# Performance work log

Measured on AMD Instinct MI355X. Metric: run time of the kernel, lower is better.

The kernel has to match this reference:

```python
import jax, jax.numpy as jnp
import numpy as np
from jax import lax

B, S, D, H, L = 2, 2048, 512, 512, 2
M, NC, K, NH, WIN = 64, 16, 4, 8, 256
MAX_LR = 0.1


def setup_inputs() -> dict:
    key = jax.random.key(0)
    keys = iter(jax.random.split(key, 40))
    def nrm(shape, scale=0.02):
        return jax.random.normal(next(keys), shape, dtype=jnp.float32) * scale
    p = {}
    p['x'] = jax.random.normal(next(keys), (B, S, D), dtype=jnp.float32)
    p['meta_memory'] = nrm((M, D), 0.05)
    p['mem_w_in'] = nrm((D, H)); p['mem_b_in'] = jnp.zeros((H,))
    p['mem_w_h'] = nrm((L, H, H)); p['mem_b_h'] = jnp.zeros((L, H))
    p['mem_w_out'] = nrm((H, D)); p['mem_b_out'] = jnp.zeros((D,))
    for n in ('w_in', 'b_in', 'w_h', 'b_h', 'w_out', 'b_out'):
        p['mom_' + n] = jnp.zeros_like(p['mem_' + n])
    for pre in ('q', 'k', 'v'):
        p[pre + '_w'] = nrm((D, D)); p[pre + '_b'] = jnp.zeros((D,))
        p[pre + '_conv'] = nrm((D, 1, K), 0.1)
    for pre in ('lr', 'fg', 'mo'):
        p[pre + '_w'] = nrm((D, 1)); p[pre + '_b'] = jnp.zeros((1,))
    for n in ('swa_wq', 'swa_wk', 'swa_wv', 'swa_wo'):
        p[n] = nrm((D, D))
    for n in ('swa_bq', 'swa_bk', 'swa_bv', 'swa_bo'):
        p[n] = jnp.zeros((D,))
    return p


def l2n(x):
    # F.normalize(x, dim=-1): x / max(||x||_2, 1e-12)
    return x / jnp.maximum(jnp.linalg.norm(x, axis=-1, keepdims=True), 1e-12)


def causal_dwconv(x, kernel):
    # x [B,S,D], kernel [D,1,K] depthwise causal conv along S
    xc = jnp.transpose(x, (0, 2, 1))  # [B,D,S]
    y = lax.conv_general_dilated(xc, kernel, window_strides=(1,), padding=[(K - 1, 0)],
                                 feature_group_count=D, dimension_numbers=('NCH', 'OIH', 'NCH'))
    return jnp.transpose(y, (0, 2, 1))


def lin_proj(x, W, b, conv, n_chunks):
    # Linear -> causal depthwise conv -> SiLU -> chunk: [B, n_chunks, S/n_chunks, D]
    y = jax.nn.silu(causal_dwconv(x @ W + b, conv))
    Bx, Sx, Dx = y.shape
    return y.reshape(Bx, n_chunks, Sx // n_chunks, Dx)


def adaptive(x, W, b, max_w):
    # data-dependent scalar gate in (0, max_w], chunked: [B, NC, chunk_len, 1]
    y = jax.nn.sigmoid(x @ W + b) * max_w
    Bx, Sx, _ = y.shape
    return y.reshape(Bx, NC, Sx // NC, 1)


def mlp(params, x):
    # ResLinear: in-proj + SiLU, residual SiLU hidden layers, out-proj
    h = jax.nn.silu(x @ params['w_in'] + params['b_in'])
    def body(h, wb):
        w, b = wb
        return h + jax.nn.silu(h @ w + b), None
    h, _ = lax.scan(body, h, (params['w_h'], params['b_h']))
    return h @ params['w_out'] + params['b_out']


def swa_attn(x, wq, bq, wk, bk, wv, bv, wo, bo):
    Bx, Sx, Dx = x.shape
    hd = Dx // NH
    def split(y):
        return jnp.transpose(y.reshape(Bx, Sx, NH, hd), (0, 2, 1, 3))
    q, k, v = split(x @ wq + bq), split(x @ wk + bk), split(x @ wv + bv)
    scores = jnp.einsum('bhqd,bhkd->bhqk', q, k) / np.sqrt(hd).astype(np.float32)
    i = jnp.arange(Sx)[:, None]
    j = jnp.arange(Sx)[None, :]
    mask = (j <= i) & (i - j < WIN)  # causal sliding window
    attn = jax.nn.softmax(jnp.where(mask, scores, jnp.float32(-1e9)), axis=-1)
    out = jnp.einsum('bhqk,bhkd->bhqd', attn, v)
    out = jnp.transpose(out, (0, 2, 1, 3)).reshape(Bx, Sx, Dx)
    return out @ wo + bo


def reference(x, meta_memory, mem_w_in, mem_b_in, mem_w_h, mem_b_h, mem_w_out, mem_b_out,
              mom_w_in, mom_b_in, mom_w_h, mom_b_h, mom_w_out, mom_b_out,
              q_w, q_b, q_conv, k_w, k_b, k_conv, v_w, v_b, v_conv,
              lr_w, lr_b, fg_w, fg_b, mo_w, mo_b,
              swa_wq, swa_bq, swa_wk, swa_bk, swa_wv, swa_bv, swa_wo, swa_bo):
    Bx = x.shape[0]
    # inject meta memory; (M+S) chosen divisible by NC so no padding branch
    xm = jnp.concatenate([jnp.broadcast_to(meta_memory, (Bx, M, D)), x], axis=1)
    q = l2n(lin_proj(xm, q_w, q_b, q_conv, 1))      # [B,1,M+S,D]
    k = l2n(lin_proj(xm, k_w, k_b, k_conv, NC))     # [B,NC,C,D]
    v = lin_proj(xm, v_w, v_b, v_conv, NC)
    lr = adaptive(xm, lr_w, lr_b, MAX_LR)           # [B,NC,C,1]
    fg = adaptive(xm, fg_w, fg_b, 1.0)
    mo = adaptive(xm, mo_w, mo_b, 1.0)
    params = {'w_in': mem_w_in, 'b_in': mem_b_in, 'w_h': mem_w_h, 'b_h': mem_b_h,
              'w_out': mem_w_out, 'b_out': mem_b_out}
    moms = {'w_in': mom_w_in, 'b_in': mom_b_in, 'w_h': mom_w_h, 'b_h': mom_b_h,
            'w_out': mom_w_out, 'b_out': mom_b_out}

    def loss_fn(p, kc, vc, lrc):
        preds = mlp(p, kc)                           # [B,C,D]
        loss = jnp.mean((preds - vc) ** 2, axis=-1)  # [B,C]
        return jnp.sum(loss * lrc[..., 0]), loss

    grads, _ = jax.vmap(jax.grad(loss_fn, has_aux=True), in_axes=(None, 1, 1, 1))(params, k, v, lr)
    alpha = fg.mean(axis=(1, 2, 3))  # [B]
    theta = lr.mean(axis=(1, 2, 3))
    eta = mo.mean(axis=(1, 2, 3))
    new_params = {}
    for name, p_ in params.items():
        g = grads[name].mean(axis=0)                # mean over chunks
        sh = (-1,) + (1,) * g.ndim                  # flatten_and_expand
        mom_b = eta.reshape(sh) * moms[name] - theta.reshape(sh) * g   # [B,*shape]
        # torch updates param.data under no_grad -> stop_gradient for faithfulness
        new_params[name] = lax.stop_gradient((p_ * (1.0 - alpha.reshape(sh)) + mom_b).mean(axis=0))
    retrieved = jax.nn.silu(mlp(new_params, q[:, 0]))
    out = swa_attn(retrieved, swa_wq, swa_bq, swa_wk, swa_bk, swa_wv, swa_bv, swa_wo, swa_bo)
    return out[:, M:, :]
```

## Files before the change

### kernel.cpp

```cpp
#include <hip/hip_runtime.h>
#include <cmath>


namespace {

constexpr int Bb   = 2;
constexpr int Ss   = 2048;
constexpr int Dd   = 512;
constexpr int Mm   = 64;
constexpr int NCc  = 16;
constexpr int NHh  = 8;
constexpr int HD   = 64;
constexpr int WINw = 256;
constexpr int Nn   = Mm + Ss;
constexpr int Rr   = Bb * Nn;
constexpr int NBD  = Rr * Dd;
constexpr float MAXLR = 0.1f;
constexpr float GS   = 256.0f;

typedef __attribute__((ext_vector_type(8))) short short8;
typedef __attribute__((ext_vector_type(8))) _Float16 half8;
typedef __attribute__((ext_vector_type(4))) float f32x4;

__device__ __forceinline__ float sigf(float x)  { return 1.0f / (1.0f + __expf(-x)); }
__device__ __forceinline__ float siluf(float x) { return x * sigf(x); }
__device__ __forceinline__ float dsiluf(float x){ float s = sigf(x); return s * (1.0f + x * (1.0f - s)); }
__device__ __forceinline__ unsigned short f2h(float f) {
    _Float16 h = (_Float16)f;
    return *(unsigned short*)&h;
}
__device__ __forceinline__ float h2f(unsigned short u) {
    return (float)(*(_Float16*)&u);
}
// ... 73 lines not shown
        unsigned short nh16[16];
        #pragma unroll
        for (int e = 0; e < 16; ++e) nh16[e] = f2h(vals[e]);
        unsigned short* np = wc.nh[seg] + (size_t)(r0 + tr) * 512 + c0 + tc;
        *(short8*)np = *(short8*)nh16; *(short8*)(np + 8) = *(short8*)(nh16 + 8);
    }
    __syncthreads();
    int c = threadIdx.x >> 2, rb = (threadIdx.x & 3) * 16;
    unsigned short o16[16];
    #pragma unroll
    for (int e = 0; e < 16; ++e) o16[e] = f2h(T[rb + e][c]);
    unsigned short* tp = wc.th[seg] + (size_t)(c0 + c) * 512 + r0 + rb;
    *(short8*)tp = *(short8*)o16; *(short8*)(tp + 8) = *(short8*)(o16 + 8);
}

struct TriW { const unsigned short* bh; const float* bias; float* c; };
struct TriSet { TriW t[3]; };

template<int TA, int TB, bool SPLITK, int EPI, bool MULTI, bool AF32>
__global__ __launch_bounds__(256) void k_mm(
        const void* Ap, const unsigned short* Bh_,
        float* C, const float* bias, const float* __restrict__ exf,
        const unsigned short* __restrict__ exh,
        const float* __restrict__ lrp,
        unsigned short* oh, TriSet ts,
        int Md, int Nd, int Kd, int accum) {
    __shared__ char smem[16384];
    unsigned short* AH = (unsigned short*)smem;
    unsigned short* BH = AH + 4096;
    const int tid = threadIdx.x;
    const int m0 = blockIdx.x * 64, n0 = blockIdx.y * 64;
    if constexpr (MULTI) {
        const TriW& tw = ts.t[blockIdx.z];
        Bh_ = tw.bh; bias = tw.bias; C = tw.c;
    }
    int kbg = 0, ke = Kd;
    if constexpr (SPLITK) {
        int kc = Kd / gridDim.z;
        kbg = blockIdx.z * kc; ke = kbg + kc;
        C += (size_t)blockIdx.z * Md * Nd;
    }
    const int astr = (TA == 0) ? Kd : Md;

    f32x4 acc[2][2];
    #pragma unroll
    for (int i = 0; i < 2; ++i)
        #pragma unroll
        for (int j = 0; j < 2; ++j)
            #pragma unroll
            for (int v = 0; v < 4; ++v) acc[i][j][v] = 0.f;

    short8 pA0, pA1, pB0, pB1;
    float4 pAf[4];

    auto gload = [&](int k0) {
        if constexpr (TA == 0) {
            int r = tid >> 2, ks2 = (tid & 3) * 16;
            if constexpr (AF32) {
                const float* ap = (const float*)Ap + (size_t)(m0 + r) * astr + k0 + ks2;
                pAf[0] = *(const float4*)ap;       pAf[1] = *(const float4*)(ap + 4);
                pAf[2] = *(const float4*)(ap + 8); pAf[3] = *(const float4*)(ap + 12);
            } else {
                const unsigned short* ah = (const unsigned short*)Ap + (size_t)(m0 + r) * astr + k0 + ks2;
                pA0 = *(const short8*)ah; pA1 = *(const short8*)(ah + 8);
            }
        } else {
            int kr = tid >> 2, ms = (tid & 3) * 16;
            const unsigned short* ah = (const unsigned short*)Ap + (size_t)(k0 + kr) * astr + m0 + ms;
            pA0 = *(const short8*)ah; pA1 = *(const short8*)(ah + 8);
        }
        if constexpr (TB == 0) {
            int nr = tid >> 2, ks2 = (tid & 3) * 16;
            const unsigned short* bh = Bh_ + (size_t)(n0 + nr) * Kd + k0 + ks2;
            pB0 = *(const short8*)bh; pB1 = *(const short8*)(bh + 8);
        } else {
            int kr = tid >> 2, nseg = (tid & 3) * 16;
            const unsigned short* bh = Bh_ + (size_t)(k0 + kr) * Nd + n0 + nseg;
            pB0 = *(const short8*)bh; pB1 = *(const short8*)(bh + 8);
        }
    };
    auto lstore = [&]() {
        if constexpr (TA == 0) {
            int r = tid >> 2, ks2 = (tid & 3) * 16;
            int f = r >> 4, rr = r & 15, kf = ks2 >> 5, q = (ks2 >> 3) & 3;
            int F = (f * 2 + kf) * 4 + q;
            int u0 = swz(F * 16 + rr) * 8, u1 = swz((F + 1) * 16 + rr) * 8;
            if constexpr (AF32) {
                unsigned short hh[16];
                const float* pf = (const float*)pAf;
                #pragma unroll
                for (int e = 0; e < 16; ++e) hh[e] = f2h(pf[e]);
                *(short8*)(AH + u0) = *(short8*)hh;  *(short8*)(AH + u1) = *(short8*)(hh + 8);
            } else {
                *(short8*)(AH + u0) = pA0; *(short8*)(AH + u1) = pA1;
            }
        } else {
            int kr = tid >> 2, ms = (tid & 3) * 16;
            int f = ms >> 4, kf = kr >> 5, q = (kr >> 3) & 3, kk = kr & 7;
            int F = (f * 2 + kf) * 4 + q;
            unsigned short tmp[16];
            *(short8*)tmp = pA0; *(short8*)(tmp + 8) = pA1;
            #pragma unroll
            for (int e = 0; e < 16; ++e) AH[swz((F << 4) | e) * 8 + kk] = tmp[e];
        }
        if constexpr (TB == 0) {
            int nr = tid >> 2, ks2 = (tid & 3) * 16;
            int f = nr >> 4, rr = nr & 15, kf = ks2 >> 5, q = (ks2 >> 3) & 3;
            int F = (f * 2 + kf) * 4 + q;
            int u0 = swz(F * 16 + rr) * 8, u1 = swz((F + 1) * 16 + rr) * 8;
            *(short8*)(BH + u0) = pB0; *(short8*)(BH + u1) = pB1;
        } else {
            int kr = tid >> 2, nseg = (tid & 3) * 16;
            int f = nseg >> 4, kf = kr >> 5, q = (kr >> 3) & 3, kk = kr & 7;
            int F = (f * 2 + kf) * 4 + q;
            unsigned short tmp[16];
            *(short8*)tmp = pB0; *(short8*)(tmp + 8) = pB1;
            #pragma unroll
            for (int e = 0; e < 16; ++e) BH[swz((F << 4) | e) * 8 + kk] = tmp[e];
        }
    };

    const int wv = tid >> 6, lr16 = tid & 15, lq = (tid >> 4) & 3;
    const int wm = wv & 1, wn = wv >> 1;

    gload(kbg); lstore();
    __syncthreads();
    for (int k0 = kbg; k0 < ke; k0 += 64) {
        bool more = (k0 + 64) < ke;
        if (more) gload(k0 + 64);
        #pragma unroll
        for (int kf = 0; kf < 2; ++kf) {
            half8 fa[2], fb[2];
            #pragma unroll
            for (int i = 0; i < 2; ++i) {
                int u = swz((((wm * 2 + i) * 2 + kf) * 4 + lq) * 16 + lr16);
                fa[i] = *(const half8*)(AH + u * 8);
            }
            #pragma unroll
            for (int j = 0; j < 2; ++j) {
                int u = swz((((wn * 2 + j) * 2 + kf) * 4 + lq) * 16 + lr16);
                fb[j] = *(const half8*)(BH + u * 8);
            }
            #pragma unroll
            for (int i = 0; i < 2; ++i)
                #pragma unroll
                for (int j = 0; j < 2; ++j)
                    acc[i][j] = __builtin_amdgcn_mfma_f32_16x16x32_f16(fa[i], fb[j], acc[i][j], 0, 0, 0);
        }
        if (more) { __syncthreads(); lstore(); __syncthreads(); }
    }
    __syncthreads();

    float* EP = (float*)smem;
    #pragma unroll
    for (int i = 0; i < 2; ++i)
        #pragma unroll
// ... 4 lines not shown
                int col = wn * 32 + j * 16 + lr16;
                int u = col >> 2, up = u ^ (row & 15);
                EP[row * 64 + up * 4 + (col & 3)] = acc[i][j][v];
            }
    __syncthreads();
    int r = tid >> 2, cg = tid & 3;
    float vv[16];
    #pragma unroll
    for (int uu = 0; uu < 4; ++uu) {
        int u = cg * 4 + uu;
        *(float4*)&vv[uu * 4] = *(const float4*)&EP[r * 64 + ((u ^ (r & 15)) * 4)];
    }
    int m = m0 + r, nb = n0 + cg * 16;
    size_t idx = (size_t)m * Nd + nb;

    if constexpr (SPLITK) {
        #pragma unroll
        for (int uu = 0; uu < 4; ++uu) *(float4*)(C + idx + uu * 4) = *(float4*)&vv[uu * 4];
        return;
    }
    if (bias) {
        #pragma unroll
        for (int uu = 0; uu < 4; ++uu) {
            float4 b4 = *(const float4*)(bias + nb + uu * 4);
            vv[uu * 4 + 0] += b4.x; vv[uu * 4 + 1] += b4.y;
            vv[uu * 4 + 2] += b4.z; vv[uu * 4 + 3] += b4.w;
        }
    }
    unsigned short eh8[16];
    if constexpr (EPI == 2 || EPI == 3 || EPI == 6) {
        #pragma unroll
        for (int k4 = 0; k4 < 2; ++k4)
            *(short8*)&eh8[k4 * 8] = *(const short8*)(exh + idx + k4 * 8);
    }
    auto store_h = [&](const float* s) {
        unsigned short hb[16];
        #pragma unroll
        for (int e = 0; e < 16; ++e) hb[e] = f2h(s[e]);
        *(short8*)(oh + idx) = *(short8*)hb;
        *(short8*)(oh + idx + 8) = *(short8*)(hb + 8);
    };
    auto accum_add = [&]() {
        #pragma unroll
        for (int uu = 0; uu < 4; ++uu) {
            float4 o4 = *(const float4*)(C + idx + uu * 4);
            vv[uu * 4 + 0] += o4.x; vv[uu * 4 + 1] += o4.y;
            vv[uu * 4 + 2] += o4.z; vv[uu * 4 + 3] += o4.w;
        }
    };
    auto store_f = [&]() {
        #pragma unroll
        for (int uu = 0; uu < 4; ++uu) *(float4*)(C + idx + uu * 4) = *(float4*)&vv[uu * 4];
    };
    if constexpr (EPI == 0) {
        if (accum) accum_add();
        store_f();
    } else if constexpr (EPI == 1) {
        float s[16];
        #pragma unroll
        for (int e = 0; e < 16; ++e) s[e] = siluf(vv[e]);
        store_h(s);
    } else if constexpr (EPI == 2) {
        float s[16];
        #pragma unroll
        for (int e = 0; e < 16; ++e) s[e] = h2f(eh8[e]) + siluf(vv[e]);
        store_h(s);
    } else if constexpr (EPI == 3) {
        float sc = GS * (2.0f / 512.0f) * lrp[m];
        float s[16];
        #pragma unroll
        for (int e = 0; e < 16; ++e) s[e] = sc * (vv[e] - h2f(eh8[e]));
        store_h(s);
    } else if constexpr (EPI == 4) {
        if (accum) accum_add();
        store_f();
        float s[16];
        #pragma unroll
        for (int e = 0; e < 16; ++e) s[e] = vv[e] * dsiluf(exf[idx + e]);
        store_h(s);
    } else if constexpr (EPI == 5) {
        store_f();
        float s[16];
        #pragma unroll
        for (int e = 0; e < 16; ++e) s[e] = siluf(vv[e]);
        store_h(s);
    } else if constexpr (EPI == 6) {
        store_f();
        float s[16];
        #pragma unroll
        for (int e = 0; e < 16; ++e) s[e] = h2f(eh8[e]) + siluf(vv[e]);
        store_h(s);
    } else if constexpr (EPI == 7) {
        int b2 = m / Nn, t2 = m - b2 * Nn;
        if (t2 >= Mm) {
            float* dst = C + (size_t)(b2 * Ss + (t2 - Mm)) * Nd + nb;
            #pragma unroll
            for (int uu = 0; uu < 4; ++uu) *(float4*)(dst + uu * 4) = *(float4*)&vv[uu * 4];
        }
    }
}

__global__ void k_reduce_splitk(const float* __restrict__ part, float* __restrict__ out,
                                int n, int z, float alpha) {
    int i = blockIdx.x * 256 + threadIdx.x;
    if (i >= n) return;
    float s = 0.f;
    for (int zz = 0; zz < z; ++zz) s += part[(size_t)zz * n + i];
    out[i] = alpha * s;
}

__global__ __launch_bounds__(256) void k_conv3(
        const float* __restrict__ yq, const float* __restrict__ yk, const float* __restrict__ yv,
        const float* __restrict__ cq, const float* __restrict__ ck, const float* __restrict__ cv,
        unsigned short* oq, unsigned short* ok, unsigned short* ov) {
    int which = blockIdx.y;
    const float* y  = which == 0 ? yq : which == 1 ? yk : yv;
    const float* cw = which == 0 ? cq : which == 1 ? ck : cv;
    unsigned short* oh = which == 0 ? oq : which == 1 ? ok : ov;
    bool norm = which < 2;
    int r = blockIdx.x;
    int b = r / Nn, t = r - b * Nn;
    const size_t rowbase = (size_t)r * Dd;
    float s[2];
    #pragma unroll
    for (int u = 0; u < 2; ++u) {
        int d = threadIdx.x + u * 256;
        float acc = 0.f;
        #pragma unroll
        for (int k = 0; k < 4; ++k) {
            int tt = t - 3 + k;
            if (tt >= 0) acc += y[(size_t)(b * Nn + tt) * Dd + d] * cw[d * 4 + k];
        }
        s[u] = siluf(acc);
    }
    float denom = 1.0f;
    if (norm) {
        __shared__ float wr[4];
        float v2 = s[0] * s[0] + s[1] * s[1];
        #pragma unroll
        for (int off = 32; off; off >>= 1) v2 += __shfl_xor(v2, off, 64);
        if ((threadIdx.x & 63) == 0) wr[threadIdx.x >> 6] = v2;
        __syncthreads();
        denom = fmaxf(sqrtf(wr[0] + wr[1] + wr[2] + wr[3]), 1e-12f);
    }
    oh[rowbase + threadIdx.x]       = f2h(s[0] / denom);
    oh[rowbase + threadIdx.x + 256] = f2h(s[1] / denom);
}

__global__ void k_colsum(const unsigned short* __restrict__ gh, float* __restrict__ part) {
    int col = blockIdx.x * 256 + threadIdx.x;
    int chunk = blockIdx.y;
    int r0 = chunk * (Rr / 64);
    float s = 0.f;
    for (int r = r0; r < r0 + Rr / 64; ++r) s += h2f(gh[(size_t)r * Dd + col]);
    part[chunk * Dd + col] = s;
}
__global__ void k_colsum_reduce(const float* __restrict__ part, float* __restrict__ out, float alpha) {
    int col = blockIdx.x * 256 + threadIdx.x;
    if (col >= Dd) return;
    float s = 0.f;
    for (int c = 0; c < 64; ++c) s += part[c * Dd + col];
    out[col] = alpha * s;
}

struct UpdW4 { const float* p[4]; const float* mo[4]; const float* g[4]; unsigned short* th[4]; };
__global__ __launch_bounds__(256) void k_updW(UpdW4 u, const float* __restrict__ scal) {
    __shared__ float T[64][65];
    int seg = blockIdx.z;
    int r0 = blockIdx.y * 64, c0 = blockIdx.x * 64;
    float a = 1.0f - scal[0], et = scal[2], th = scal[1];
    int tr = threadIdx.x >> 2, tc = (threadIdx.x & 3) * 16;
    size_t base = (size_t)(r0 + tr) * 512 + c0 + tc;
    #pragma unroll
    for (int q = 0; q < 4; ++q) {
        float4 p4 = *(const float4*)(u.p[seg] + base + q * 4);
        float4 m4 = *(const float4*)(u.mo[seg] + base + q * 4);
        float4 g4 = *(const float4*)(u.g[seg] + base + q * 4);
// ... 5 lines not shown
    __syncthreads();
    int c = threadIdx.x >> 2, rb = (threadIdx.x & 3) * 16;
    unsigned short o16[16];
    #pragma unroll
    for (int e = 0; e < 16; ++e) o16[e] = f2h(T[rb + e][c]);
    unsigned short* tp = u.th[seg] + (size_t)(c0 + c) * 512 + r0 + rb;
    *(short8*)tp = *(short8*)o16; *(short8*)(tp + 8) = *(short8*)(o16 + 8);
}
struct UpdB4 { const float* p[4]; const float* mo[4]; const float* g[4]; float* o[4]; };
__global__ void k_updB(UpdB4 u, const float* __restrict__ scal) {
    int seg = blockIdx.x >> 1;
    int i = (blockIdx.x & 1) * 256 + threadIdx.x;
    u.o[seg][i] = u.p[seg][i] * (1.0f - scal[0]) + scal[2] * u.mo[seg][i] - scal[1] * u.g[seg][i];
}

__global__ __launch_bounds__(256) void k_swa(const float* __restrict__ qs,
                                             const float* __restrict__ ks,
                                             const float* __restrict__ vs,
                                             float* __restrict__ out) {
    __shared__ unsigned short KH[2048], VH[2048];
    __shared__ unsigned short PH[4][512];
    const int tid = threadIdx.x;
    const int w = tid >> 6, lane = tid & 63;
    const int lq = lane >> 4, l16 = lane & 15;
    const int q0 = blockIdx.x * 64;
    const int bh = blockIdx.y;
    const int h = bh & 7, b = bh >> 3;
    const size_t srow = (size_t)(b * Nn) * Dd + h * HD;
    const int iq = q0 + w * 16 + l16;

    half8 qh[2];
    {
        const float* qr = qs + srow + (size_t)iq * Dd;
        #pragma unroll
        for (int kf = 0; kf < 2; ++kf) {
            float t8[8];
            *(float4*)&t8[0] = *(const float4*)(qr + kf * 32 + lq * 8);
            *(float4*)&t8[4] = *(const float4*)(qr + kf * 32 + lq * 8 + 4);
            unsigned short hh[8];
            #pragma unroll
            for (int e = 0; e < 8; ++e) hh[e] = f2h(t8[e]);
            qh[kf] = *(half8*)hh;
        }
    }

    f32x4 o[4];
    #pragma unroll
    for (int nf = 0; nf < 4; ++nf)
        #pragma unroll
        for (int v = 0; v < 4; ++v) o[nf][v] = 0.f;
    float mrun[4] = { -1e30f, -1e30f, -1e30f, -1e30f };
    float lrun[4] = { 0.f, 0.f, 0.f, 0.f };
    const int iw = q0 + w * 16 + lq * 4;

    int jlo = q0 - (WINw - 1); if (jlo < 0) jlo = 0;
    jlo &= ~31;
    for (int jt = jlo; jt < q0 + 64; jt += 32) {
        __syncthreads();
        {
            int nr = tid >> 3, ds8 = (tid & 7) * 8;
            const float* kr = ks + srow + (size_t)(jt + nr) * Dd + ds8;
            float t8[8];
            *(float4*)&t8[0] = *(const float4*)kr;
            *(float4*)&t8[4] = *(const float4*)(kr + 4);
            unsigned short hh[8];
            #pragma unroll
            for (int e = 0; e < 8; ++e) hh[e] = f2h(t8[e]);
            int f = nr >> 4, rr = nr & 15, kf = ds8 >> 5, q = (ds8 >> 3) & 3;
            int u = swz(((f * 2 + kf) * 4 + q) * 16 + rr);
            *(short8*)(KH + u * 8) = *(short8*)hh;
        }
        {
            int d = tid & 63, kg = tid >> 6;
            unsigned short hh[8];
            #pragma unroll
            for (int e = 0; e < 8; ++e)
                hh[e] = f2h(vs[srow + (size_t)(jt + kg * 8 + e) * Dd + d]);
            int f = d >> 4, rr = d & 15;
            int u = swz((f * 4 + kg) * 16 + rr);
            *(short8*)(VH + u * 8) = *(short8*)hh;
        }
        __syncthreads();

        f32x4 s[2];
        #pragma unroll
        for (int nf = 0; nf < 2; ++nf) {
            #pragma unroll
            for (int v = 0; v < 4; ++v) s[nf][v] = 0.f;
            #pragma unroll
            for (int kf = 0; kf < 2; ++kf) {
                int u = swz(((nf * 2 + kf) * 4 + lq) * 16 + l16);
                half8 kb = *(const half8*)(KH + u * 8);
// ... 47 lines not shown
        half8 pah = *(const half8*)(&PH[w][pa]);
        #pragma unroll
        for (int nf = 0; nf < 4; ++nf) {
            int u = swz((nf * 4 + lq) * 16 + l16);
            half8 vth = *(const half8*)(VH + u * 8);
            o[nf] = __builtin_amdgcn_mfma_f32_16x16x32_f16(pah, vth, o[nf], 0, 0, 0);
        }
    }
    float invl[4];
    #pragma unroll
    for (int v = 0; v < 4; ++v) invl[v] = 1.0f / lrun[v];
    #pragma unroll
    for (int nf = 0; nf < 4; ++nf)
        #pragma unroll
        for (int v = 0; v < 4; ++v)
            out[srow + (size_t)(iw + v) * Dd + nf * 16 + l16] = o[nf][v] * invl[v];
}

}

extern "C" void kernel_launch(void* const* d_in, const int* in_sizes, int n_in,
                              void* d_out, int out_size, void* d_ws, size_t ws_size,
                              hipStream_t stream) {
    const float* x       = (const float*)d_in[0];
    const float* meta    = (const float*)d_in[1];
    const float* mWin    = (const float*)d_in[2];
    const float* mbin    = (const float*)d_in[3];
    const float* mWh     = (const float*)d_in[4];
    const float* mbh     = (const float*)d_in[5];
    const float* mWout   = (const float*)d_in[6];
    const float* mbout   = (const float*)d_in[7];
// ... 17 lines not shown

    char* wsb = (char*)d_ws;
    size_t off = 0;
    auto allocB = [&](size_t bytes) { void* p = wsb + off; off = (off + bytes + 255) & ~(size_t)255; return p; };
    auto allocU = [&](size_t elems) { return (unsigned short*)allocB(elems * 2); };
    auto allocF = [&](size_t elems) { return (float*)allocB(elems * 4); };

    unsigned short *xm_h = allocU(NBD);
    unsigned short *qb_h = allocU(NBD);
    unsigned short *kb_h = allocU(NBD);
    unsigned short *vb_h = allocU(NBD);
    unsigned short *h0_h = allocU(NBD);
    unsigned short *h1_h = allocU(NBD);
    unsigned short *h2_h = allocU(NBD);
    unsigned short *g1_h = allocU(NBD);
    float *f0 = allocF(NBD), *f1 = allocF(NBD), *f2 = allocF(NBD), *f3 = allocF(NBD);
    float *parts = allocF((size_t)12 * 262144);
    const int WEL = 262144;
    unsigned short *wt_h[11], *wn_h[11];
    for (int i = 0; i < 11; ++i) { wt_h[i] = allocU(WEL); wn_h[i] = nullptr; }
    for (int i = 8; i < 11; ++i) wn_h[i] = allocU(WEL);
    unsigned short *nWinT_h = allocU(WEL);
    unsigned short *nWh0T_h = allocU(WEL);
    unsigned short *nWh1T_h = allocU(WEL);
    unsigned short *nWoutT_h = allocU(WEL);
    float *gWin = allocF(WEL), *gWh0 = allocF(WEL), *gWh1 = allocF(WEL), *gWout = allocF(WEL);
    float *gbin = allocF(512), *gbh0 = allocF(512), *gbh1 = allocF(512), *gbout = allocF(512);
    float *nbin = allocF(512), *nbh0 = allocF(512), *nbh1 = allocF(512), *nbout = allocF(512);
    float *lr_t = allocF(Rr), *fg_t = allocF(Rr), *mo_t = allocF(Rr);
    float *scal = allocF(8);
    float *cpart = allocF(64 * 512);
    unsigned short *gA_h = vb_h;
    unsigned short *gB_h = xm_h;

    TriSet none{};
    const dim3 GG(66, 8);
    const float GALPHA = 1.0f / (NCc * GS);

    WC wc{};
    const float* wlist[11] = { q_w, k_w, v_w, swa_wq, swa_wk, swa_wv, swa_wo,
                               mWin, mWh, mWh + WEL, mWout };
    for (int i = 0; i < 11; ++i) { wc.w[i] = wlist[i]; wc.th[i] = wt_h[i]; wc.nh[i] = wn_h[i]; }
    k_wconv<<<dim3(8, 8, 11), 256, 0, stream>>>(wc);

    k_build_xm<<<(Rr * 128 + 255) / 256, 256, 0, stream>>>(x, meta, xm_h);
    k_gates<<<Rr / 4, 256, 0, stream>>>(xm_h, lr_w, lr_b, fg_w, fg_b, mo_w, mo_b, lr_t, fg_t, mo_t);
    k_gate_means<<<1, 256, 0, stream>>>(lr_t, fg_t, mo_t, scal);

    TriSet qkvA{{ { wt_h[0], q_b, f0 }, { wt_h[1], k_b, f1 }, { wt_h[2], v_b, f2 } }};
    k_mm<0, 0, false, 0, true, false><<<dim3(66, 8, 3), 256, 0, stream>>>(
        xm_h, nullptr, nullptr, nullptr, nullptr, nullptr, nullptr, nullptr, qkvA, Rr, Dd, Dd, 0);
    k_conv3<<<dim3(Rr, 3), 256, 0, stream>>>(f0, f1, f2, q_c, k_c, v_c, qb_h, kb_h, vb_h);

    k_mm<0, 0, false, 5, false, false><<<GG, 256, 0, stream>>>(
        kb_h, wt_h[7], f0, mbin, nullptr, nullptr, nullptr, h0_h, none, Rr, Dd, Dd, 0);
    k_mm<0, 0, false, 6, false, false><<<GG, 256, 0, stream>>>(
        h0_h, wt_h[8], f1, mbh, nullptr, h0_h, nullptr, h1_h, none, Rr, Dd, Dd, 0);
    k_mm<0, 0, false, 6, false, false><<<GG, 256, 0, stream>>>(
        h1_h, wt_h[9], f2, mbh + 512, nullptr, h1_h, nullptr, h2_h, none, Rr, Dd, Dd, 0);
    k_mm<0, 0, false, 3, false, false><<<GG, 256, 0, stream>>>(
        h2_h, wt_h[10], nullptr, mbout, nullptr, vb_h, lr_t, g1_h, none, Rr, Dd, Dd, 0);

    auto GRADW = [&](const unsigned short* ah, const unsigned short* bh, float* gout) {
        k_mm<1, 1, true, 0, false, false><<<dim3(8, 8, 11), 256, 0, stream>>>(
            ah, bh, parts, nullptr, nullptr, nullptr, nullptr, nullptr, none, Dd, Dd, Rr, 0);
        k_reduce_splitk<<<1024, 256, 0, stream>>>(parts, gout, WEL, 11, GALPHA);
    };
    auto COLSUM = [&](const unsigned short* gh, float* bo) {
        k_colsum<<<dim3(2, 64), 256, 0, stream>>>(gh, cpart);
        k_colsum_reduce<<<2, 256, 0, stream>>>(cpart, bo, GALPHA);
    };
    GRADW(h2_h, g1_h, gWout);  COLSUM(g1_h, gbout);
    k_mm<0, 0, false, 4, false, false><<<GG, 256, 0, stream>>>(
        g1_h, wn_h[10], f3, nullptr, f2, nullptr, nullptr, gA_h, none, Rr, Dd, Dd, 0);
    GRADW(h1_h, gA_h, gWh1);   COLSUM(gA_h, gbh1);
    k_mm<0, 0, false, 4, false, false><<<GG, 256, 0, stream>>>(
        gA_h, wn_h[9], f3, nullptr, f1, nullptr, nullptr, gB_h, none, Rr, Dd, Dd, 1);
    GRADW(h0_h, gB_h, gWh0);   COLSUM(gB_h, gbh0);
    k_mm<0, 0, false, 4, false, false><<<GG, 256, 0, stream>>>(
        gB_h, wn_h[8], f3, nullptr, f0, nullptr, nullptr, gA_h, none, Rr, Dd, Dd, 1);
    GRADW(kb_h, gA_h, gWin);   COLSUM(gA_h, gbin);

    UpdW4 uw{ { mWin, mWh, mWh + WEL, mWout },
              { momWin, momWh, momWh + WEL, momWout },
              { gWin, gWh0, gWh1, gWout },
              { nWinT_h, nWh0T_h, nWh1T_h, nWoutT_h } };
    k_updW<<<dim3(8, 8, 4), 256, 0, stream>>>(uw, scal);
    UpdB4 ub{ { mbin, mbh, mbh + 512, mbout },
              { mombin, mombh, mombh + 512, mombout },
              { gbin, gbh0, gbh1, gbout },
              { nbin, nbh0, nbh1, nbout } };
    k_updB<<<8, 256, 0, stream>>>(ub, scal);

    k_mm<0, 0, false, 1, false, false><<<GG, 256, 0, stream>>>(
        qb_h, nWinT_h, nullptr, nbin, nullptr, nullptr, nullptr, g1_h, none, Rr, Dd, Dd, 0);
    k_mm<0, 0, false, 2, false, false><<<GG, 256, 0, stream>>>(
        g1_h, nWh0T_h, nullptr, nbh0, nullptr, g1_h, nullptr, h0_h, none, Rr, Dd, Dd, 0);
    k_mm<0, 0, false, 2, false, false><<<GG, 256, 0, stream>>>(
        h0_h, nWh1T_h, nullptr, nbh1, nullptr, h0_h, nullptr, h1_h, none, Rr, Dd, Dd, 0);
    k_mm<0, 0, false, 1, false, false><<<GG, 256, 0, stream>>>(
        h1_h, nWoutT_h, nullptr, nbout, nullptr, nullptr, nullptr, h2_h, none, Rr, Dd, Dd, 0);

    TriSet qkvF{{ { wt_h[3], swa_bq, f0 }, { wt_h[4], swa_bk, f1 }, { wt_h[5], swa_bv, f2 } }};
    k_mm<0, 0, false, 0, true, false><<<dim3(66, 8, 3), 256, 0, stream>>>(
        h2_h, nullptr, nullptr, nullptr, nullptr, nullptr, nullptr, nullptr, qkvF, Rr, Dd, Dd, 0);
    k_swa<<<dim3(Nn / 64, Bb * NHh), 256, 0, stream>>>(f0, f1, f2, f3);
    k_mm<0, 0, false, 7, false, true><<<GG, 256, 0, stream>>>(
        f3, wt_h[6], (float*)d_out, swa_bo, nullptr, nullptr, nullptr, nullptr, none, Rr, Dd, Dd, 0);
}
```

Measured before the change: 512.5 us.

## Store intermediates in fp16, batch weight-gradient GEMMs, load B fragments directly

```diff
diff --git a/kernel.cpp b/kernel.cpp
--- a/kernel.cpp
+++ b/kernel.cpp
@@ -17,6 +17,7 @@
 constexpr int NBD  = Rr * Dd;
 constexpr float MAXLR = 0.1f;
 constexpr float GS   = 256.0f;
+constexpr int WEL  = 262144;
 
 typedef __attribute__((ext_vector_type(8))) short short8;
 typedef __attribute__((ext_vector_type(8))) _Float16 half8;
@@ -120,16 +121,18 @@
     *(short8*)tp = *(short8*)o16; *(short8*)(tp + 8) = *(short8*)(o16 + 8);
 }
 
-struct TriW { const unsigned short* bh; const float* bias; float* c; };
+struct TriW { const unsigned short* bh; const float* bias; unsigned short* ch; };
 struct TriSet { TriW t[3]; };
-
-template<int TA, int TB, bool SPLITK, int EPI, bool MULTI, bool AF32>
+struct Grad4 { const unsigned short* a[4]; const unsigned short* b[4]; };
+
+template<int TA, int TB, bool SPLITK, int EPI, bool MULTI, bool GRAD4>
 __global__ __launch_bounds__(256) void k_mm(
-        const void* Ap, const unsigned short* Bh_,
-        float* C, const float* bias, const float* __restrict__ exf,
-        const unsigned short* __restrict__ exh,
+        const unsigned short* Ap, const unsigned short* Bh_,
+        float* C, const float* bias,
+        const unsigned short* __restrict__ exA,
+        const unsigned short* __restrict__ exD,
         const float* __restrict__ lrp,
-        unsigned short* oh, TriSet ts,
+        unsigned short* oh, unsigned short* oh2, TriSet ts, Grad4 g4,
         int Md, int Nd, int Kd, int accum) {
     __shared__ char smem[16384];
     unsigned short* AH = (unsigned short*)smem;
@@ -138,10 +141,15 @@
     const int m0 = blockIdx.x * 64, n0 = blockIdx.y * 64;
     if constexpr (MULTI) {
         const TriW& tw = ts.t[blockIdx.z];
-        Bh_ = tw.bh; bias = tw.bias; C = tw.c;
+        Bh_ = tw.bh; bias = tw.bias; oh = tw.ch;
     }
     int kbg = 0, ke = Kd;
-    if constexpr (SPLITK) {
+    if constexpr (GRAD4) {
+        int seg = blockIdx.z / 11, kz = blockIdx.z - seg * 11;
+        kbg = kz * 384; ke = kbg + 384;
+        C += (size_t)blockIdx.z * Md * Nd;
+        Ap = g4.a[seg]; Bh_ = g4.b[seg];
+    } else if constexpr (SPLITK) {
         int kc = Kd / gridDim.z;
         kbg = blockIdx.z * kc; ke = kbg + kc;
         C += (size_t)blockIdx.z * Md * Nd;
@@ -157,29 +165,24 @@
             for (int v = 0; v < 4; ++v) acc[i][j][v] = 0.f;
 
     short8 pA0, pA1, pB0, pB1;
-    float4 pAf[4];
+
+    const int wv = tid >> 6, lr16 = tid & 15, lq = (tid >> 4) & 3;
+    const int wm = wv & 1, wn = wv >> 1;
+    const unsigned short* bdir = nullptr;
+    if constexpr (TB == 0)
+        bdir = Bh_ + (size_t)(n0 + wn * 32 + lr16) * Kd + lq * 8;
 
     auto gload = [&](int k0) {
         if constexpr (TA == 0) {
             int r = tid >> 2, ks2 = (tid & 3) * 16;
-            if constexpr (AF32) {
-                const float* ap = (const float*)Ap + (size_t)(m0 + r) * astr + k0 + ks2;
-                pAf[0] = *(const float4*)ap;       pAf[1] = *(const float4*)(ap + 4);
-                pAf[2] = *(const float4*)(ap + 8); pAf[3] = *(const float4*)(ap + 12);
-            } else {
-                const unsigned short* ah = (const unsigned short*)Ap + (size_t)(m0 + r) * astr + k0 + ks2;
-                pA0 = *(const short8*)ah; pA1 = *(const short8*)(ah + 8);
-            }
+            const unsigned short* ah = Ap + (size_t)(m0 + r) * astr + k0 + ks2;
+            pA0 = *(const short8*)ah; pA1 = *(const short8*)(ah + 8);
         } else {
             int kr = tid >> 2, ms = (tid & 3) * 16;
-            const unsigned short* ah = (const unsigned short*)Ap + (size_t)(k0 + kr) * astr + m0 + ms;
+            const unsigned short* ah = Ap + (size_t)(k0 + kr) * astr + m0 + ms;
             pA0 = *(const short8*)ah; pA1 = *(const short8*)(ah + 8);
         }
-        if constexpr (TB == 0) {
-            int nr = tid >> 2, ks2 = (tid & 3) * 16;
-            const unsigned short* bh = Bh_ + (size_t)(n0 + nr) * Kd + k0 + ks2;
-            pB0 = *(const short8*)bh; pB1 = *(const short8*)(bh + 8);
-        } else {
+        if constexpr (TB == 1) {
             int kr = tid >> 2, nseg = (tid & 3) * 16;
             const unsigned short* bh = Bh_ + (size_t)(k0 + kr) * Nd + n0 + nseg;
             pB0 = *(const short8*)bh; pB1 = *(const short8*)(bh + 8);
@@ -191,15 +194,7 @@
             int f = r >> 4, rr = r & 15, kf = ks2 >> 5, q = (ks2 >> 3) & 3;
             int F = (f * 2 + kf) * 4 + q;
             int u0 = swz(F * 16 + rr) * 8, u1 = swz((F + 1) * 16 + rr) * 8;
-            if constexpr (AF32) {
-                unsigned short hh[16];
-                const float* pf = (const float*)pAf;
-                #pragma unroll
-                for (int e = 0; e < 16; ++e) hh[e] = f2h(pf[e]);
-                *(short8*)(AH + u0) = *(short8*)hh;  *(short8*)(AH + u1) = *(short8*)(hh + 8);
-            } else {
-                *(short8*)(AH + u0) = pA0; *(short8*)(AH + u1) = pA1;
-            }
+            *(short8*)(AH + u0) = pA0; *(short8*)(AH + u1) = pA1;
         } else {
             int kr = tid >> 2, ms = (tid & 3) * 16;
             int f = ms >> 4, kf = kr >> 5, q = (kr >> 3) & 3, kk = kr & 7;
@@ -209,13 +204,7 @@
             #pragma unroll
             for (int e = 0; e < 16; ++e) AH[swz((F << 4) | e) * 8 + kk] = tmp[e];
         }
-        if constexpr (TB == 0) {
-            int nr = tid >> 2, ks2 = (tid & 3) * 16;
-            int f = nr >> 4, rr = nr & 15, kf = ks2 >> 5, q = (ks2 >> 3) & 3;
-            int F = (f * 2 + kf) * 4 + q;
-            int u0 = swz(F * 16 + rr) * 8, u1 = swz((F + 1) * 16 + rr) * 8;
-            *(short8*)(BH + u0) = pB0; *(short8*)(BH + u1) = pB1;
-        } else {
+        if constexpr (TB == 1) {
             int kr = tid >> 2, nseg = (tid & 3) * 16;
             int f = nseg >> 4, kf = kr >> 5, q = (kr >> 3) & 3, kk = kr & 7;
             int F = (f * 2 + kf) * 4 + q;
@@ -226,14 +215,19 @@
         }
     };
 
-    const int wv = tid >> 6, lr16 = tid & 15, lq = (tid >> 4) & 3;
-    const int wm = wv & 1, wn = wv >> 1;
-
     gload(kbg); lstore();
     __syncthreads();
     for (int k0 = kbg; k0 < ke; k0 += 64) {
         bool more = (k0 + 64) < ke;
         if (more) gload(k0 + 64);
+        half8 gb[2][2];
+        if constexpr (TB == 0) {
+            #pragma unroll
+            for (int kf = 0; kf < 2; ++kf)
+                #pragma unroll
+                for (int j = 0; j < 2; ++j)
+                    gb[kf][j] = *(const half8*)(bdir + (size_t)j * 16 * Kd + k0 + kf * 32);
+        }
         #pragma unroll
         for (int kf = 0; kf < 2; ++kf) {
             half8 fa[2], fb[2];
@@ -244,8 +238,11 @@
             }
             #pragma unroll
             for (int j = 0; j < 2; ++j) {
-                int u = swz((((wn * 2 + j) * 2 + kf) * 4 + lq) * 16 + lr16);
-                fb[j] = *(const half8*)(BH + u * 8);
+                if constexpr (TB == 0) fb[j] = gb[kf][j];
+                else {
+                    int u = swz((((wn * 2 + j) * 2 + kf) * 4 + lq) * 16 + lr16);
+                    fb[j] = *(const half8*)(BH + u * 8);
+                }
             }
             #pragma unroll
             for (int i = 0; i < 2; ++i)
@@ -280,7 +277,7 @@
     int m = m0 + r, nb = n0 + cg * 16;
     size_t idx = (size_t)m * Nd + nb;
 
-    if constexpr (SPLITK) {
+    if constexpr (SPLITK || GRAD4) {
         #pragma unroll
         for (int uu = 0; uu < 4; ++uu) *(float4*)(C + idx + uu * 4) = *(float4*)&vv[uu * 4];
         return;
@@ -293,11 +290,10 @@
             vv[uu * 4 + 2] += b4.z; vv[uu * 4 + 3] += b4.w;
         }
     }
-    unsigned short eh8[16];
+    unsigned short ea[16];
     if constexpr (EPI == 2 || EPI == 3 || EPI == 6) {
-        #pragma unroll
-        for (int k4 = 0; k4 < 2; ++k4)
-            *(short8*)&eh8[k4 * 8] = *(const short8*)(exh + idx + k4 * 8);
+        *(short8*)&ea[0] = *(const short8*)(exA + idx);
+        *(short8*)&ea[8] = *(const short8*)(exA + idx + 8);
     }
     auto store_h = [&](const float* s) {
         unsigned short hb[16];
@@ -306,21 +302,24 @@
         *(short8*)(oh + idx) = *(short8*)hb;
         *(short8*)(oh + idx + 8) = *(short8*)(hb + 8);
     };
-    auto accum_add = [&]() {
-        #pragma unroll
-        for (int uu = 0; uu < 4; ++uu) {
-            float4 o4 = *(const float4*)(C + idx + uu * 4);
-            vv[uu * 4 + 0] += o4.x; vv[uu * 4 + 1] += o4.y;
-            vv[uu * 4 + 2] += o4.z; vv[uu * 4 + 3] += o4.w;
-        }
-    };
-    auto store_f = [&]() {
-        #pragma unroll
-        for (int uu = 0; uu < 4; ++uu) *(float4*)(C + idx + uu * 4) = *(float4*)&vv[uu * 4];
+    auto store_h2 = [&](const float* s) {
+        unsigned short hb[16];
+        #pragma unroll
+        for (int e = 0; e < 16; ++e) hb[e] = f2h(s[e]);
+        *(short8*)(oh2 + idx) = *(short8*)hb;
+        *(short8*)(oh2 + idx + 8) = *(short8*)(hb + 8);
     };
     if constexpr (EPI == 0) {
-        if (accum) accum_add();
-        store_f();
+        if (accum) {
+            #pragma unroll
+            for (int uu = 0; uu < 4; ++uu) {
+                float4 o4 = *(const float4*)(C + idx + uu * 4);
+                vv[uu * 4 + 0] += o4.x; vv[uu * 4 + 1] += o4.y;
+                vv[uu * 4 + 2] += o4.z; vv[uu * 4 + 3] += o4.w;
+            }
+        }
+        #pragma unroll
+        for (int uu = 0; uu < 4; ++uu) *(float4*)(C + idx + uu * 4) = *(float4*)&vv[uu * 4];
     } else if constexpr (EPI == 1) {
         float s[16];
         #pragma unroll
@@ -329,32 +328,43 @@
     } else if constexpr (EPI == 2) {
         float s[16];
         #pragma unroll
-        for (int e = 0; e < 16; ++e) s[e] = h2f(eh8[e]) + siluf(vv[e]);
+        for (int e = 0; e < 16; ++e) s[e] = h2f(ea[e]) + siluf(vv[e]);
         store_h(s);
     } else if constexpr (EPI == 3) {
         float sc = GS * (2.0f / 512.0f) * lrp[m];
         float s[16];
         #pragma unroll
-        for (int e = 0; e < 16; ++e) s[e] = sc * (vv[e] - h2f(eh8[e]));
+        for (int e = 0; e < 16; ++e) s[e] = sc * (vv[e] - h2f(ea[e]));
         store_h(s);
     } else if constexpr (EPI == 4) {
-        if (accum) accum_add();
-        store_f();
+        if (accum) {
+            #pragma unroll
+            for (int uu = 0; uu < 4; ++uu) {
+                float4 o4 = *(const float4*)(C + idx + uu * 4);
+                vv[uu * 4 + 0] += o4.x; vv[uu * 4 + 1] += o4.y;
+                vv[uu * 4 + 2] += o4.z; vv[uu * 4 + 3] += o4.w;
+            }
+        }
+        #pragma unroll
+        for (int uu = 0; uu < 4; ++uu) *(float4*)(C + idx + uu * 4) = *(float4*)&vv[uu * 4];
+        unsigned short ed[16];
+        *(short8*)&ed[0] = *(const short8*)(exD + idx);
+        *(short8*)&ed[8] = *(const short8*)(exD + idx + 8);
         float s[16];
         #pragma unroll
-        for (int e = 0; e < 16; ++e) s[e] = vv[e] * dsiluf(exf[idx + e]);
+        for (int e = 0; e < 16; ++e) s[e] = vv[e] * dsiluf(h2f(ed[e]));
         store_h(s);
     } else if constexpr (EPI == 5) {
-        store_f();
+        store_h2(vv);
         float s[16];
         #pragma unroll
         for (int e = 0; e < 16; ++e) s[e] = siluf(vv[e]);
         store_h(s);
     } else if constexpr (EPI == 6) {
-        store_f();
+        store_h2(vv);
         float s[16];
         #pragma unroll
-        for (int e = 0; e < 16; ++e) s[e] = h2f(eh8[e]) + siluf(vv[e]);
+        for (int e = 0; e < 16; ++e) s[e] = h2f(ea[e]) + siluf(vv[e]);
         store_h(s);
     } else if constexpr (EPI == 7) {
         int b2 = m / Nn, t2 = m - b2 * Nn;
@@ -363,24 +373,48 @@
             #pragma unroll
             for (int uu = 0; uu < 4; ++uu) *(float4*)(dst + uu * 4) = *(float4*)&vv[uu * 4];
         }
-    }
-}
-
-__global__ void k_reduce_splitk(const float* __restrict__ part, float* __restrict__ out,
-                                int n, int z, float alpha) {
-    int i = blockIdx.x * 256 + threadIdx.x;
-    if (i >= n) return;
+    } else if constexpr (EPI == 8) {
+        store_h(vv);
+    }
+}
+
+struct Red4 { float* o[4]; };
+__global__ void k_reduce4(const float* __restrict__ part, Red4 r, float alpha) {
+    int seg = blockIdx.x >> 10;
+    int i = (blockIdx.x & 1023) * 256 + threadIdx.x;
+    const float* p = part + (size_t)seg * 11 * WEL;
     float s = 0.f;
-    for (int zz = 0; zz < z; ++zz) s += part[(size_t)zz * n + i];
-    out[i] = alpha * s;
+    #pragma unroll
+    for (int z = 0; z < 11; ++z) s += p[(size_t)z * WEL + i];
+    r.o[seg][i] = alpha * s;
+}
+
+struct CS4 { const unsigned short* g[4]; };
+__global__ void k_colsum4(CS4 cs, float* __restrict__ part) {
+    int col = blockIdx.x * 256 + threadIdx.x;
+    int chunk = blockIdx.y, seg = blockIdx.z;
+    const unsigned short* g = cs.g[seg];
+    int r0 = chunk * (Rr / 64);
+    float s = 0.f;
+    for (int r = r0; r < r0 + Rr / 64; ++r) s += h2f(g[(size_t)r * Dd + col]);
+    part[((size_t)seg * 64 + chunk) * Dd + col] = s;
+}
+__global__ void k_colsum_red4(const float* __restrict__ part, Red4 r, float alpha) {
+    int col = blockIdx.x * 256 + threadIdx.x;
+    int seg = blockIdx.y;
+    float s = 0.f;
+    #pragma unroll
+    for (int c = 0; c < 64; ++c) s += part[((size_t)seg * 64 + c) * Dd + col];
+    r.o[seg][col] = alpha * s;
 }
 
 __global__ __launch_bounds__(256) void k_conv3(
-        const float* __restrict__ yq, const float* __restrict__ yk, const float* __restrict__ yv,
+        const unsigned short* __restrict__ yq, const unsigned short* __restrict__ yk,
+        const unsigned short* __restrict__ yv,
         const float* __restrict__ cq, const float* __restrict__ ck, const float* __restrict__ cv,
         unsigned short* oq, unsigned short* ok, unsigned short* ov) {
     int which = blockIdx.y;
-    const float* y  = which == 0 ? yq : which == 1 ? yk : yv;
+    const unsigned short* y = which == 0 ? yq : which == 1 ? yk : yv;
     const float* cw = which == 0 ? cq : which == 1 ? ck : cv;
     unsigned short* oh = which == 0 ? oq : which == 1 ? ok : ov;
     bool norm = which < 2;
@@ -395,7 +429,7 @@
         #pragma unroll
         for (int k = 0; k < 4; ++k) {
             int tt = t - 3 + k;
-            if (tt >= 0) acc += y[(size_t)(b * Nn + tt) * Dd + d] * cw[d * 4 + k];
+            if (tt >= 0) acc += h2f(y[(size_t)(b * Nn + tt) * Dd + d]) * cw[d * 4 + k];
         }
         s[u] = siluf(acc);
     }
@@ -411,22 +445,6 @@
     }
     oh[rowbase + threadIdx.x]       = f2h(s[0] / denom);
     oh[rowbase + threadIdx.x + 256] = f2h(s[1] / denom);
-}
-
-__global__ void k_colsum(const unsigned short* __restrict__ gh, float* __restrict__ part) {
-    int col = blockIdx.x * 256 + threadIdx.x;
-    int chunk = blockIdx.y;
-    int r0 = chunk * (Rr / 64);
-    float s = 0.f;
-    for (int r = r0; r < r0 + Rr / 64; ++r) s += h2f(gh[(size_t)r * Dd + col]);
-    part[chunk * Dd + col] = s;
-}
-__global__ void k_colsum_reduce(const float* __restrict__ part, float* __restrict__ out, float alpha) {
-    int col = blockIdx.x * 256 + threadIdx.x;
-    if (col >= Dd) return;
-    float s = 0.f;
-    for (int c = 0; c < 64; ++c) s += part[c * Dd + col];
-    out[col] = alpha * s;
 }
 
 struct UpdW4 { const float* p[4]; const float* mo[4]; const float* g[4]; unsigned short* th[4]; };
@@ -462,10 +480,10 @@
     u.o[seg][i] = u.p[seg][i] * (1.0f - scal[0]) + scal[2] * u.mo[seg][i] - scal[1] * u.g[seg][i];
 }
 
-__global__ __launch_bounds__(256) void k_swa(const float* __restrict__ qs,
-                                             const float* __restrict__ ks,
-                                             const float* __restrict__ vs,
-                                             float* __restrict__ out) {
+__global__ __launch_bounds__(256) void k_swa(const unsigned short* __restrict__ qs,
+                                             const unsigned short* __restrict__ ks,
+                                             const unsigned short* __restrict__ vs,
+                                             unsigned short* __restrict__ out) {
     __shared__ unsigned short KH[2048], VH[2048];
     __shared__ unsigned short PH[4][512];
     const int tid = threadIdx.x;
@@ -479,17 +497,9 @@
 
     half8 qh[2];
     {
-        const float* qr = qs + srow + (size_t)iq * Dd;
-        #pragma unroll
-        for (int kf = 0; kf < 2; ++kf) {
-            float t8[8];
-            *(float4*)&t8[0] = *(const float4*)(qr + kf * 32 + lq * 8);
-            *(float4*)&t8[4] = *(const float4*)(qr + kf * 32 + lq * 8 + 4);
-            unsigned short hh[8];
-            #pragma unroll
-            for (int e = 0; e < 8; ++e) hh[e] = f2h(t8[e]);
-            qh[kf] = *(half8*)hh;
-        }
+        const unsigned short* qr = qs + srow + (size_t)iq * Dd;
+        qh[0] = *(const half8*)(qr + lq * 8);
+        qh[1] = *(const half8*)(qr + 32 + lq * 8);
     }
 
     f32x4 o[4];
@@ -507,23 +517,17 @@
         __syncthreads();
         {
             int nr = tid >> 3, ds8 = (tid & 7) * 8;
-            const float* kr = ks + srow + (size_t)(jt + nr) * Dd + ds8;
-            float t8[8];
-            *(float4*)&t8[0] = *(const float4*)kr;
-            *(float4*)&t8[4] = *(const float4*)(kr + 4);
-            unsigned short hh[8];
-            #pragma unroll
-            for (int e = 0; e < 8; ++e) hh[e] = f2h(t8[e]);
+            short8 kv = *(const short8*)(ks + srow + (size_t)(jt + nr) * Dd + ds8);
             int f = nr >> 4, rr = nr & 15, kf = ds8 >> 5, q = (ds8 >> 3) & 3;
             int u = swz(((f * 2 + kf) * 4 + q) * 16 + rr);
-            *(short8*)(KH + u * 8) = *(short8*)hh;
+            *(short8*)(KH + u * 8) = kv;
         }
         {
             int d = tid & 63, kg = tid >> 6;
             unsigned short hh[8];
             #pragma unroll
             for (int e = 0; e < 8; ++e)
-                hh[e] = f2h(vs[srow + (size_t)(jt + kg * 8 + e) * Dd + d]);
+                hh[e] = vs[srow + (size_t)(jt + kg * 8 + e) * Dd + d];
             int f = d >> 4, rr = d & 15;
             int u = swz((f * 4 + kg) * 16 + rr);
             *(short8*)(VH + u * 8) = *(short8*)hh;
@@ -601,7 +605,7 @@
     for (int nf = 0; nf < 4; ++nf)
         #pragma unroll
         for (int v = 0; v < 4; ++v)
-            out[srow + (size_t)(iw + v) * Dd + nf * 16 + l16] = o[nf][v] * invl[v];
+            out[srow + (size_t)(iw + v) * Dd + nf * 16 + l16] = f2h(o[nf][v] * invl[v]);
 }
 
 }
@@ -649,9 +653,12 @@
     unsigned short *h1_h = allocU(NBD);
     unsigned short *h2_h = allocU(NBD);
     unsigned short *g1_h = allocU(NBD);
-    float *f0 = allocF(NBD), *f1 = allocF(NBD), *f2 = allocF(NBD), *f3 = allocF(NBD);
-    float *parts = allocF((size_t)12 * 262144);
-    const int WEL = 262144;
+    unsigned short *z0p  = allocU(NBD);
+    unsigned short *a0p  = allocU(NBD);
+    unsigned short *a1p  = allocU(NBD);
+    unsigned short *da0  = allocU(NBD);
+    float *f3 = allocF(NBD);
+    float *parts = allocF((size_t)44 * WEL);
     unsigned short *wt_h[11], *wn_h[11];
     for (int i = 0; i < 11; ++i) { wt_h[i] = allocU(WEL); wn_h[i] = nullptr; }
     for (int i = 8; i < 11; ++i) wn_h[i] = allocU(WEL);
@@ -664,11 +671,12 @@
     float *nbin = allocF(512), *nbh0 = allocF(512), *nbh1 = allocF(512), *nbout = allocF(512);
     float *lr_t = allocF(Rr), *fg_t = allocF(Rr), *mo_t = allocF(Rr);
     float *scal = allocF(8);
-    float *cpart = allocF(64 * 512);
-    unsigned short *gA_h = vb_h;
-    unsigned short *gB_h = xm_h;
-
-    TriSet none{};
+    float *cpart = allocF(4 * 64 * 512);
+    unsigned short *da1 = xm_h;
+    unsigned short *dz0 = vb_h;
+    unsigned short *soh = kb_h;
+
+    TriSet none{}; Grad4 g0{};
     const dim3 GG(66, 8);
     const float GALPHA = 1.0f / (NCc * GS);
 
@@ -682,39 +690,37 @@
     k_gates<<<Rr / 4, 256, 0, stream>>>(xm_h, lr_w, lr_b, fg_w, fg_b, mo_w, mo_b, lr_t, fg_t, mo_t);
     k_gate_means<<<1, 256, 0, stream>>>(lr_t, fg_t, mo_t, scal);
 
-    TriSet qkvA{{ { wt_h[0], q_b, f0 }, { wt_h[1], k_b, f1 }, { wt_h[2], v_b, f2 } }};
-    k_mm<0, 0, false, 0, true, false><<<dim3(66, 8, 3), 256, 0, stream>>>(
-        xm_h, nullptr, nullptr, nullptr, nullptr, nullptr, nullptr, nullptr, qkvA, Rr, Dd, Dd, 0);
-    k_conv3<<<dim3(Rr, 3), 256, 0, stream>>>(f0, f1, f2, q_c, k_c, v_c, qb_h, kb_h, vb_h);
+    TriSet qkvA{{ { wt_h[0], q_b, h0_h }, { wt_h[1], k_b, h1_h }, { wt_h[2], v_b, h2_h } }};
+    k_mm<0, 0, false, 8, true, false><<<dim3(66, 8, 3), 256, 0, stream>>>(
+        xm_h, nullptr, nullptr, nullptr, nullptr, nullptr, nullptr, nullptr, nullptr,
+        qkvA, g0, Rr, Dd, Dd, 0);
+    k_conv3<<<dim3(Rr, 3), 256, 0, stream>>>(h0_h, h1_h, h2_h, q_c, k_c, v_c, qb_h, kb_h, vb_h);
 
     k_mm<0, 0, false, 5, false, false><<<GG, 256, 0, stream>>>(
-        kb_h, wt_h[7], f0, mbin, nullptr, nullptr, nullptr, h0_h, none, Rr, Dd, Dd, 0);
+        kb_h, wt_h[7], nullptr, mbin, nullptr, nullptr, nullptr, h0_h, z0p, none, g0, Rr, Dd, Dd, 0);
     k_mm<0, 0, false, 6, false, false><<<GG, 256, 0, stream>>>(
-        h0_h, wt_h[8], f1, mbh, nullptr, h0_h, nullptr, h1_h, none, Rr, Dd, Dd, 0);
+        h0_h, wt_h[8], nullptr, mbh, h0_h, nullptr, nullptr, h1_h, a0p, none, g0, Rr, Dd, Dd, 0);
     k_mm<0, 0, false, 6, false, false><<<GG, 256, 0, stream>>>(
-        h1_h, wt_h[9], f2, mbh + 512, nullptr, h1_h, nullptr, h2_h, none, Rr, Dd, Dd, 0);
+        h1_h, wt_h[9], nullptr, mbh + 512, h1_h, nullptr, nullptr, h2_h, a1p, none, g0, Rr, Dd, Dd, 0);
     k_mm<0, 0, false, 3, false, false><<<GG, 256, 0, stream>>>(
-        h2_h, wt_h[10], nullptr, mbout, nullptr, vb_h, lr_t, g1_h, none, Rr, Dd, Dd, 0);
-
-    auto GRADW = [&](const unsigned short* ah, const unsigned short* bh, float* gout) {
-        k_mm<1, 1, true, 0, false, false><<<dim3(8, 8, 11), 256, 0, stream>>>(
-            ah, bh, parts, nullptr, nullptr, nullptr, nullptr, nullptr, none, Dd, Dd, Rr, 0);
-        k_reduce_splitk<<<1024, 256, 0, stream>>>(parts, gout, WEL, 11, GALPHA);
-    };
-    auto COLSUM = [&](const unsigned short* gh, float* bo) {
-        k_colsum<<<dim3(2, 64), 256, 0, stream>>>(gh, cpart);
-        k_colsum_reduce<<<2, 256, 0, stream>>>(cpart, bo, GALPHA);
-    };
-    GRADW(h2_h, g1_h, gWout);  COLSUM(g1_h, gbout);
+        h2_h, wt_h[10], nullptr, mbout, vb_h, nullptr, lr_t, g1_h, nullptr, none, g0, Rr, Dd, Dd, 0);
+
     k_mm<0, 0, false, 4, false, false><<<GG, 256, 0, stream>>>(
-        g1_h, wn_h[10], f3, nullptr, f2, nullptr, nullptr, gA_h, none, Rr, Dd, Dd, 0);
-    GRADW(h1_h, gA_h, gWh1);   COLSUM(gA_h, gbh1);
+        g1_h, wn_h[10], f3, nullptr, nullptr, a1p, nullptr, da1, nullptr, none, g0, Rr, Dd, Dd, 0);
     k_mm<0, 0, false, 4, false, false><<<GG, 256, 0, stream>>>(
-        gA_h, wn_h[9], f3, nullptr, f1, nullptr, nullptr, gB_h, none, Rr, Dd, Dd, 1);
-    GRADW(h0_h, gB_h, gWh0);   COLSUM(gB_h, gbh0);
+        da1, wn_h[9], f3, nullptr, nullptr, a0p, nullptr, da0, nullptr, none, g0, Rr, Dd, Dd, 1);
     k_mm<0, 0, false, 4, false, false><<<GG, 256, 0, stream>>>(
-        gB_h, wn_h[8], f3, nullptr, f0, nullptr, nullptr, gA_h, none, Rr, Dd, Dd, 1);
-    GRADW(kb_h, gA_h, gWin);   COLSUM(gA_h, gbin);
+        da0, wn_h[8], f3, nullptr, nullptr, z0p, nullptr, dz0, nullptr, none, g0, Rr, Dd, Dd, 1);
+    Grad4 g4{{ h2_h, h1_h, h0_h, kb_h }, { g1_h, da1, da0, dz0 }};
+    k_mm<1, 1, true, 0, false, true><<<dim3(8, 8, 44), 256, 0, stream>>>(
+        nullptr, nullptr, parts, nullptr, nullptr, nullptr, nullptr, nullptr, nullptr,
+        none, g4, Dd, Dd, Rr, 0);
+    Red4 rw{{ gWout, gWh1, gWh0, gWin }};
+    k_reduce4<<<4096, 256, 0, stream>>>(parts, rw, GALPHA);
+    CS4 cs{{ g1_h, da1, da0, dz0 }};
+    k_colsum4<<<dim3(2, 64, 4), 256, 0, stream>>>(cs, cpart);
+    Red4 rb{{ gbout, gbh1, gbh0, gbin }};
+    k_colsum_red4<<<dim3(2, 4), 256, 0, stream>>>(cpart, rb, GALPHA);
 
     UpdW4 uw{ { mWin, mWh, mWh + WEL, mWout },
               { momWin, momWh, momWh + WEL, momWout },
@@ -728,18 +734,20 @@
     k_updB<<<8, 256, 0, stream>>>(ub, scal);
 
     k_mm<0, 0, false, 1, false, false><<<GG, 256, 0, stream>>>(
-        qb_h, nWinT_h, nullptr, nbin, nullptr, nullptr, nullptr, g1_h, none, Rr, Dd, Dd, 0);
+        qb_h, nWinT_h, nullptr, nbin, nullptr, nullptr, nullptr, g1_h, nullptr, none, g0, Rr, Dd, Dd, 0);
     k_mm<0, 0, false, 2, false, false><<<GG, 256, 0, stream>>>(
-        g1_h, nWh0T_h, nullptr, nbh0, nullptr, g1_h, nullptr, h0_h, none, Rr, Dd, Dd, 0);
+        g1_h, nWh0T_h, nullptr, nbh0, g1_h, nullptr, nullptr, h0_h, nullptr, none, g0, Rr, Dd, Dd, 0);
     k_mm<0, 0, false, 2, false, false><<<GG, 256, 0, stream>>>(
-        h0_h, nWh1T_h, nullptr, nbh1, nullptr, h0_h, nullptr, h1_h, none, Rr, Dd, Dd, 0);
+        h0_h, nWh1T_h, nullptr, nbh1, h0_h, nullptr, nullptr, h1_h, nullptr, none, g0, Rr, Dd, Dd, 0);
     k_mm<0, 0, false, 1, false, false><<<GG, 256, 0, stream>>>(
-        h1_h, nWoutT_h, nullptr, nbout, nullptr, nullptr, nullptr, h2_h, none, Rr, Dd, Dd, 0);
-
-    TriSet qkvF{{ { wt_h[3], swa_bq, f0 }, { wt_h[4], swa_bk, f1 }, { wt_h[5], swa_bv, f2 } }};
-    k_mm<0, 0, false, 0, true, false><<<dim3(66, 8, 3), 256, 0, stream>>>(
-        h2_h, nullptr, nullptr, nullptr, nullptr, nullptr, nullptr, nullptr, qkvF, Rr, Dd, Dd, 0);
-    k_swa<<<dim3(Nn / 64, Bb * NHh), 256, 0, stream>>>(f0, f1, f2, f3);
-    k_mm<0, 0, false, 7, false, true><<<GG, 256, 0, stream>>>(
-        f3, wt_h[6], (float*)d_out, swa_bo, nullptr, nullptr, nullptr, nullptr, none, Rr, Dd, Dd, 0);
-}
+        h1_h, nWoutT_h, nullptr, nbout, nullptr, nullptr, nullptr, h2_h, nullptr, none, g0, Rr, Dd, Dd, 0);
+
+    TriSet qkvF{{ { wt_h[3], swa_bq, z0p }, { wt_h[4], swa_bk, a0p }, { wt_h[5], swa_bv, a1p } }};
+    k_mm<0, 0, false, 8, true, false><<<dim3(66, 8, 3), 256, 0, stream>>>(
+        h2_h, nullptr, nullptr, nullptr, nullptr, nullptr, nullptr, nullptr, nullptr,
+        qkvF, g0, Rr, Dd, Dd, 0);
+    k_swa<<<dim3(Nn / 64, Bb * NHh), 256, 0, stream>>>(z0p, a0p, a1p, soh);
+    k_mm<0, 0, false, 7, false, false><<<GG, 256, 0, stream>>>(
+        soh, wt_h[6], (float*)d_out, swa_bo, nullptr, nullptr, nullptr, nullptr, nullptr,
+        none, g0, Rr, Dd, Dd, 0);
+}
```

New measurement: 547.8 us. 6.9% more time.
